# Kernel tuning notes

Measured on AMD Instinct MI355X. Metric: run time of the kernel, lower is better.

The kernel has to match this reference:

```python
import jax, jax.numpy as jnp
import numpy as np

BETA = 0.5
THRESHOLD = 1.0
SLOPE = 25.0  # fast_sigmoid surrogate slope
NUM_STEPS, BATCH = 80, 65536
NUM_INPUTS, NUM_HIDDEN, NUM_OUTPUTS = 20, 10, 2


@jax.custom_vjp
def spike_fn(x):
    # Heaviside fire: spk = 1 if (mem - threshold) > 0
    return (x > 0).astype(x.dtype)

def _spike_fwd(x):
    return spike_fn(x), x

def _spike_bwd(x, g):
    # snntorch surrogate.fast_sigmoid(slope=25): grad = 1/(slope*|x|+1)^2
    return (g / (SLOPE * jnp.abs(x) + 1.0) ** 2,)

spike_fn.defvjp(_spike_fwd, _spike_bwd)


def setup_inputs() -> dict:
    key = jax.random.key(0)
    kx, k1, k2, k3, k4 = jax.random.split(key, 5)
    x = jax.random.normal(kx, (NUM_STEPS, BATCH, NUM_INPUTS), dtype=jnp.float32)
    # nn.Linear-style init: U(-1/sqrt(fan_in), 1/sqrt(fan_in))
    b1_lim = 1.0 / np.sqrt(NUM_INPUTS)
    b2_lim = 1.0 / np.sqrt(NUM_HIDDEN)
    W1 = jax.random.uniform(k1, (NUM_HIDDEN, NUM_INPUTS), jnp.float32, -b1_lim, b1_lim)
    b1 = jax.random.uniform(k2, (NUM_HIDDEN,), jnp.float32, -b1_lim, b1_lim)
    W2 = jax.random.uniform(k3, (NUM_OUTPUTS, NUM_HIDDEN), jnp.float32, -b2_lim, b2_lim)
    b2 = jax.random.uniform(k4, (NUM_OUTPUTS,), jnp.float32, -b2_lim, b2_lim)
    return {"x": x, "W1": W1, "b1": b1, "W2": W2, "b2": b2}


def reference(x, W1, b1, W2, b2):
    B = x.shape[1]
    mem1_0 = jnp.zeros((B, NUM_HIDDEN), dtype=x.dtype)
    mem2_0 = jnp.zeros((B, NUM_OUTPUTS), dtype=x.dtype)

    def step(carry, x_t):
        mem1, mem2 = carry
        # layer 1: Linear + Leaky (reset_mechanism='subtract')
        cur1 = x_t @ W1.T + b1                      # [B, 10]
        reset1 = spike_fn(mem1 - THRESHOLD)         # spike of previous mem
        mem1 = BETA * mem1 + cur1 - reset1 * THRESHOLD
        spk1 = spike_fn(mem1 - THRESHOLD)
        # layer 2
        cur2 = spk1 @ W2.T + b2                     # [B, 2]
        reset2 = spike_fn(mem2 - THRESHOLD)
        mem2 = BETA * mem2 + cur2 - reset2 * THRESHOLD
        spk2 = spike_fn(mem2 - THRESHOLD)
        return (mem1, mem2), (spk2, mem2)

    _, (spk2_rec, mem2_rec) = jax.lax.scan(step, (mem1_0, mem2_0), x)
    return spk2_rec, mem2_rec  # each [80, B, 2]
```

## Files before the change

kernel.cpp:

```cpp
#include <hip/hip_runtime.h>

#define NSTEPS 80
#define BATCH  65536
#define NIN    20
#define NHID   10
#define NOUT   2

__device__ __forceinline__ void load_x20(float* __restrict__ dst,
                                         const float* __restrict__ src) {
#pragma unroll
  for (int k = 0; k < NIN; k += 4) {
    const float4 v = *reinterpret_cast<const float4*>(src + k);
    dst[k + 0] = v.x; dst[k + 1] = v.y; dst[k + 2] = v.z; dst[k + 3] = v.w;
  }
}

__device__ __forceinline__ void st_nt2(float* p, float2 v) {
  union { float2 f; double d; } u; u.f = v;
  __builtin_nontemporal_store(u.d, reinterpret_cast<double*>(p));
}

__device__ __forceinline__ void snn_step(
    const float (&xb)[NIN],
    const float (&w1)[NHID][NIN], const float (&bb1)[NHID],
    const float (&w2)[NOUT][NHID], const float (&bb2)[NOUT],
    float (&mem1)[NHID], float (&mem2)[NOUT],
    float2& spk_out, float2& mem_out)
{
  float spk1[NHID];
#pragma unroll
  for (int j = 0; j < NHID; ++j) {
    float acc = 0.0f;
#pragma unroll
    for (int k = 0; k < NIN; ++k) acc = fmaf(xb[k], w1[j][k], acc);
    const float cur = acc + bb1[j];
    const float reset = (mem1[j] >= 1.0f) ? 1.0f : 0.0f;
    const float m = fmaf(0.5f, mem1[j], cur) - reset;
    mem1[j] = m;
    spk1[j] = (m >= 1.0f) ? 1.0f : 0.0f;
  }
#pragma unroll
  for (int o = 0; o < NOUT; ++o) {
    float acc = 0.0f;
#pragma unroll
    for (int j = 0; j < NHID; ++j) acc = fmaf(spk1[j], w2[o][j], acc);
    const float cur = acc + bb2[o];
    const float reset = (mem2[o] >= 1.0f) ? 1.0f : 0.0f;
    mem2[o] = fmaf(0.5f, mem2[o], cur) - reset;
  }
  spk_out = make_float2((mem2[0] >= 1.0f) ? 1.0f : 0.0f,
                        (mem2[1] >= 1.0f) ? 1.0f : 0.0f);
  mem_out = make_float2(mem2[0], mem2[1]);
}

__global__ __launch_bounds__(256, 1)
void snn_forward(const float* __restrict__ x,
                 const float* __restrict__ W1, const float* __restrict__ B1,
                 const float* __restrict__ W2, const float* __restrict__ B2,
                 float* __restrict__ out)
{
  const int b = blockIdx.x * blockDim.x + threadIdx.x;

  float w1[NHID][NIN];
#pragma unroll
  for (int j = 0; j < NHID; ++j)
#pragma unroll
    for (int k = 0; k < NIN; k += 4) {
      const float4 v = *reinterpret_cast<const float4*>(W1 + j * NIN + k);
      w1[j][k] = v.x; w1[j][k + 1] = v.y; w1[j][k + 2] = v.z; w1[j][k + 3] = v.w;
    }
  float bb1[NHID];
#pragma unroll
  for (int j = 0; j < NHID; ++j) bb1[j] = B1[j];
  float w2[NOUT][NHID];
#pragma unroll
  for (int o = 0; o < NOUT; ++o)
#pragma unroll
    for (int j = 0; j < NHID; ++j) w2[o][j] = W2[o * NHID + j];
  float bb2[NOUT];
#pragma unroll
  for (int o = 0; o < NOUT; ++o) bb2[o] = B2[o];

  float mem1[NHID];
#pragma unroll
  for (int j = 0; j < NHID; ++j) mem1[j] = 0.0f;
  float mem2[NOUT] = {0.0f, 0.0f};

  const size_t ss = (size_t)BATCH * NIN;
  const size_t os = (size_t)BATCH * NOUT;
  const float* xp = x + (size_t)b * NIN;
  float* sp = out + (size_t)b * NOUT;
  float* mp = sp + (size_t)NSTEPS * BATCH * NOUT;

  float B0[NIN], B1b[NIN], B2b[NIN], B3[NIN];
  load_x20(B0,  xp);
  load_x20(B1b, xp + 1 * ss);
  load_x20(B2b, xp + 2 * ss);

#define SNN_STEP_EMIT(BUF)                                          \
  {                                                                 \
    float2 s_, m_;                                                  \
    snn_step(BUF, w1, bb1, w2, bb2, mem1, mem2, s_, m_);            \
    st_nt2(sp, s_); st_nt2(mp, m_);                                 \
    sp += os; mp += os;                                             \
  }

  for (int t = 0; t < NSTEPS; t += 4) {
    if (t + 3 < NSTEPS) load_x20(B3,  xp + (size_t)(t + 3) * ss);
    SNN_STEP_EMIT(B0);
    if (t + 4 < NSTEPS) load_x20(B0,  xp + (size_t)(t + 4) * ss);
    SNN_STEP_EMIT(B1b);
    if (t + 5 < NSTEPS) load_x20(B1b, xp + (size_t)(t + 5) * ss);
    SNN_STEP_EMIT(B2b);
    if (t + 6 < NSTEPS) load_x20(B2b, xp + (size_t)(t + 6) * ss);
    SNN_STEP_EMIT(B3);
  }
#undef SNN_STEP_EMIT
}

extern "C" void kernel_launch(void* const* d_in, const int* in_sizes, int n_in,
                              void* d_out, int out_size, void* d_ws, size_t ws_size,
                              hipStream_t stream) {
  (void)in_sizes; (void)n_in; (void)d_ws; (void)ws_size; (void)out_size;
  const float* x  = (const float*)d_in[0];
  const float* W1 = (const float*)d_in[1];
  const float* B1 = (const float*)d_in[2];
  const float* W2 = (const float*)d_in[3];
  const float* B2 = (const float*)d_in[4];
  float* out = (float*)d_out;

  dim3 grid(BATCH / 256), block(256);
  snn_forward<<<grid, block, 0, stream>>>(x, W1, B1, W2, B2, out);
}
```

Before: 104.4 us.

## Split hidden neurons across lane pairs to double thread count

Each batch element is now handled by two adjacent lanes, each computing five of the ten hidden neurons, exchanging spikes via a lane shuffle. Each lane writes either the spike or membrane output. Doubles the grid and allows two blocks per CU, with a three-buffer prefetch instead of four, to improve latency hiding. Both lanes redundantly load the full input row, and a shuffle per step is added.

```diff
diff --git a/kernel.cpp b/kernel.cpp
--- a/kernel.cpp
+++ b/kernel.cpp
@@ -5,6 +5,7 @@
 #define NIN    20
 #define NHID   10
 #define NOUT   2
+#define NH2    5
 
 __device__ __forceinline__ void load_x20(float* __restrict__ dst,
                                          const float* __restrict__ src) {
@@ -20,30 +21,38 @@
   __builtin_nontemporal_store(u.d, reinterpret_cast<double*>(p));
 }
 
-__device__ __forceinline__ void snn_step(
-    const float (&xb)[NIN],
-    const float (&w1)[NHID][NIN], const float (&bb1)[NHID],
+__device__ __forceinline__ void snn_step2(
+    const float (&xb)[NIN], int h,
+    const float (&w1)[NH2][NIN], const float (&bb1)[NH2],
     const float (&w2)[NOUT][NHID], const float (&bb2)[NOUT],
-    float (&mem1)[NHID], float (&mem2)[NOUT],
+    float (&mem1)[NH2], float (&mem2)[NOUT],
     float2& spk_out, float2& mem_out)
 {
-  float spk1[NHID];
+  float a[NH2];
 #pragma unroll
-  for (int j = 0; j < NHID; ++j) {
+  for (int jj = 0; jj < NH2; ++jj) {
     float acc = 0.0f;
 #pragma unroll
-    for (int k = 0; k < NIN; ++k) acc = fmaf(xb[k], w1[j][k], acc);
-    const float cur = acc + bb1[j];
-    const float reset = (mem1[j] >= 1.0f) ? 1.0f : 0.0f;
-    const float m = fmaf(0.5f, mem1[j], cur) - reset;
-    mem1[j] = m;
-    spk1[j] = (m >= 1.0f) ? 1.0f : 0.0f;
+    for (int k = 0; k < NIN; ++k) acc = fmaf(xb[k], w1[jj][k], acc);
+    const float cur = acc + bb1[jj];
+    const float reset = (mem1[jj] >= 1.0f) ? 1.0f : 0.0f;
+    const float m = fmaf(0.5f, mem1[jj], cur) - reset;
+    mem1[jj] = m;
+    a[jj] = (m >= 1.0f) ? 1.0f : 0.0f;
   }
+  float o5[NH2];
+#pragma unroll
+  for (int jj = 0; jj < NH2; ++jj) o5[jj] = __shfl_xor(a[jj], 1);
+  float s[NHID];
+#pragma unroll
+  for (int j = 0; j < NH2; ++j)  s[j]       = h ? o5[j] : a[j];
+#pragma unroll
+  for (int j = 0; j < NH2; ++j)  s[NH2 + j] = h ? a[j]  : o5[j];
 #pragma unroll
   for (int o = 0; o < NOUT; ++o) {
     float acc = 0.0f;
 #pragma unroll
-    for (int j = 0; j < NHID; ++j) acc = fmaf(spk1[j], w2[o][j], acc);
+    for (int j = 0; j < NHID; ++j) acc = fmaf(s[j], w2[o][j], acc);
     const float cur = acc + bb2[o];
     const float reset = (mem2[o] >= 1.0f) ? 1.0f : 0.0f;
     mem2[o] = fmaf(0.5f, mem2[o], cur) - reset;
@@ -53,25 +62,28 @@
   mem_out = make_float2(mem2[0], mem2[1]);
 }
 
-__global__ __launch_bounds__(256, 1)
-void snn_forward(const float* __restrict__ x,
-                 const float* __restrict__ W1, const float* __restrict__ B1,
-                 const float* __restrict__ W2, const float* __restrict__ B2,
-                 float* __restrict__ out)
+__global__ __launch_bounds__(256, 2)
+void snn_forward2(const float* __restrict__ x,
+                  const float* __restrict__ W1, const float* __restrict__ B1,
+                  const float* __restrict__ W2, const float* __restrict__ B2,
+                  float* __restrict__ out)
 {
-  const int b = blockIdx.x * blockDim.x + threadIdx.x;
+  const int i = blockIdx.x * blockDim.x + threadIdx.x;
+  const int b = i >> 1;
+  const int h = i & 1;
+  const int j0 = NH2 * h;
 
-  float w1[NHID][NIN];
+  float w1[NH2][NIN];
 #pragma unroll
-  for (int j = 0; j < NHID; ++j)
+  for (int jj = 0; jj < NH2; ++jj)
 #pragma unroll
     for (int k = 0; k < NIN; k += 4) {
-      const float4 v = *reinterpret_cast<const float4*>(W1 + j * NIN + k);
-      w1[j][k] = v.x; w1[j][k + 1] = v.y; w1[j][k + 2] = v.z; w1[j][k + 3] = v.w;
+      const float4 v = *reinterpret_cast<const float4*>(W1 + (j0 + jj) * NIN + k);
+      w1[jj][k] = v.x; w1[jj][k + 1] = v.y; w1[jj][k + 2] = v.z; w1[jj][k + 3] = v.w;
     }
-  float bb1[NHID];
+  float bb1[NH2];
 #pragma unroll
-  for (int j = 0; j < NHID; ++j) bb1[j] = B1[j];
+  for (int jj = 0; jj < NH2; ++jj) bb1[jj] = B1[j0 + jj];
   float w2[NOUT][NHID];
 #pragma unroll
   for (int o = 0; o < NOUT; ++o)
@@ -81,40 +93,38 @@
 #pragma unroll
   for (int o = 0; o < NOUT; ++o) bb2[o] = B2[o];
 
-  float mem1[NHID];
+  float mem1[NH2];
 #pragma unroll
-  for (int j = 0; j < NHID; ++j) mem1[j] = 0.0f;
+  for (int jj = 0; jj < NH2; ++jj) mem1[jj] = 0.0f;
   float mem2[NOUT] = {0.0f, 0.0f};
 
   const size_t ss = (size_t)BATCH * NIN;
   const size_t os = (size_t)BATCH * NOUT;
   const float* xp = x + (size_t)b * NIN;
-  float* sp = out + (size_t)b * NOUT;
-  float* mp = sp + (size_t)NSTEPS * BATCH * NOUT;
+  float* op = out + (h ? (size_t)NSTEPS * BATCH * NOUT : 0) + (size_t)b * NOUT;
 
-  float B0[NIN], B1b[NIN], B2b[NIN], B3[NIN];
-  load_x20(B0,  xp);
-  load_x20(B1b, xp + 1 * ss);
-  load_x20(B2b, xp + 2 * ss);
+  float A[NIN], Bb[NIN], C[NIN];
+  load_x20(A,  xp);
+  load_x20(Bb, xp + ss);
 
-#define SNN_STEP_EMIT(BUF)                                          \
-  {                                                                 \
-    float2 s_, m_;                                                  \
-    snn_step(BUF, w1, bb1, w2, bb2, mem1, mem2, s_, m_);            \
-    st_nt2(sp, s_); st_nt2(mp, m_);                                 \
-    sp += os; mp += os;                                             \
+#define SNN_STEP_EMIT(BUF)                                           \
+  {                                                                  \
+    float2 s_, m_;                                                   \
+    snn_step2(BUF, h, w1, bb1, w2, bb2, mem1, mem2, s_, m_);         \
+    st_nt2(op, h ? m_ : s_);                                         \
+    op += os;                                                        \
   }
 
-  for (int t = 0; t < NSTEPS; t += 4) {
-    if (t + 3 < NSTEPS) load_x20(B3,  xp + (size_t)(t + 3) * ss);
-    SNN_STEP_EMIT(B0);
-    if (t + 4 < NSTEPS) load_x20(B0,  xp + (size_t)(t + 4) * ss);
-    SNN_STEP_EMIT(B1b);
-    if (t + 5 < NSTEPS) load_x20(B1b, xp + (size_t)(t + 5) * ss);
-    SNN_STEP_EMIT(B2b);
-    if (t + 6 < NSTEPS) load_x20(B2b, xp + (size_t)(t + 6) * ss);
-    SNN_STEP_EMIT(B3);
+  for (int t = 0; t < 78; t += 3) {
+    load_x20(C,  xp + (size_t)(t + 2) * ss);
+    SNN_STEP_EMIT(A);
+    load_x20(A,  xp + (size_t)(t + 3) * ss);
+    SNN_STEP_EMIT(Bb);
+    load_x20(Bb, xp + (size_t)(t + 4) * ss);
+    SNN_STEP_EMIT(C);
   }
+  SNN_STEP_EMIT(A);
+  SNN_STEP_EMIT(Bb);
 #undef SNN_STEP_EMIT
 }
 
@@ -129,6 +139,6 @@
   const float* B2 = (const float*)d_in[4];
   float* out = (float*)d_out;
 
-  dim3 grid(BATCH / 256), block(256);
-  snn_forward<<<grid, block, 0, stream>>>(x, W1, B1, W2, B2, out);
+  dim3 grid(2 * BATCH / 256), block(256);
+  snn_forward2<<<grid, block, 0, stream>>>(x, W1, B1, W2, B2, out);
 }
```

Measured after the change: 99.92 us. -4.3%, faster.

## Split each batch row across a quad of lanes with shuffle-based exchange

Applied to the files above, without the earlier changes.

Each batch element is now handled by four lanes. Each lane loads a float4 slice of the input, and the quad all-gathers the slices via xor shuffles. Each lane computes three of the ten hidden neurons and the spikes are exchanged by shuffles. Moving W1 into shared memory, giving each lane fewer registers and launching four times as many threads are meant to raise occupancy and memory-level parallelism. In exchange, the shuffles and the layer-2 computation are duplicated across the quad, and lane q==0 does extra work on the tail elements.

```diff
diff --git a/kernel.cpp b/kernel.cpp
--- a/kernel.cpp
+++ b/kernel.cpp
@@ -6,116 +6,161 @@
 #define NHID   10
 #define NOUT   2
 
-__device__ __forceinline__ void load_x20(float* __restrict__ dst,
-                                         const float* __restrict__ src) {
-#pragma unroll
-  for (int k = 0; k < NIN; k += 4) {
-    const float4 v = *reinterpret_cast<const float4*>(src + k);
-    dst[k + 0] = v.x; dst[k + 1] = v.y; dst[k + 2] = v.z; dst[k + 3] = v.w;
-  }
-}
-
 __device__ __forceinline__ void st_nt2(float* p, float2 v) {
   union { float2 f; double d; } u; u.f = v;
   __builtin_nontemporal_store(u.d, reinterpret_cast<double*>(p));
 }
 
-__device__ __forceinline__ void snn_step(
-    const float (&xb)[NIN],
-    const float (&w1)[NHID][NIN], const float (&bb1)[NHID],
-    const float (&w2)[NOUT][NHID], const float (&bb2)[NOUT],
-    float (&mem1)[NHID], float (&mem2)[NOUT],
-    float2& spk_out, float2& mem_out)
-{
-  float spk1[NHID];
+__device__ __constant__ int c_row0[4] = {0, 3, 6, 8};
+
+__device__ __forceinline__ void quad_allgather4(float (&G)[4][4],
+                                                const float4 V, int q) {
+  float v[4] = {V.x, V.y, V.z, V.w};
+  float u[4], p[4], w[4];
 #pragma unroll
-  for (int j = 0; j < NHID; ++j) {
-    float acc = 0.0f;
+  for (int c = 0; c < 4; ++c) u[c] = __shfl_xor(v[c], 1);
 #pragma unroll
-    for (int k = 0; k < NIN; ++k) acc = fmaf(xb[k], w1[j][k], acc);
-    const float cur = acc + bb1[j];
-    const float reset = (mem1[j] >= 1.0f) ? 1.0f : 0.0f;
-    const float m = fmaf(0.5f, mem1[j], cur) - reset;
-    mem1[j] = m;
-    spk1[j] = (m >= 1.0f) ? 1.0f : 0.0f;
+  for (int c = 0; c < 4; ++c) p[c] = __shfl_xor(v[c], 2);
+#pragma unroll
+  for (int c = 0; c < 4; ++c) w[c] = __shfl_xor(u[c], 2);
+#pragma unroll
+  for (int a = 0; a < 4; ++a) {
+#pragma unroll
+    for (int c = 0; c < 4; ++c) {
+      const int m = q ^ a;
+      G[a][c] = (m == 0) ? v[c] : (m == 1) ? u[c] : (m == 2) ? p[c] : w[c];
+    }
   }
-#pragma unroll
-  for (int o = 0; o < NOUT; ++o) {
-    float acc = 0.0f;
-#pragma unroll
-    for (int j = 0; j < NHID; ++j) acc = fmaf(spk1[j], w2[o][j], acc);
-    const float cur = acc + bb2[o];
-    const float reset = (mem2[o] >= 1.0f) ? 1.0f : 0.0f;
-    mem2[o] = fmaf(0.5f, mem2[o], cur) - reset;
-  }
-  spk_out = make_float2((mem2[0] >= 1.0f) ? 1.0f : 0.0f,
-                        (mem2[1] >= 1.0f) ? 1.0f : 0.0f);
-  mem_out = make_float2(mem2[0], mem2[1]);
 }
 
-__global__ __launch_bounds__(256, 1)
-void snn_forward(const float* __restrict__ x,
-                 const float* __restrict__ W1, const float* __restrict__ B1,
-                 const float* __restrict__ W2, const float* __restrict__ B2,
-                 float* __restrict__ out)
+__global__ __launch_bounds__(256, 4)
+void snn_forward4(const float* __restrict__ x,
+                  const float* __restrict__ W1, const float* __restrict__ B1,
+                  const float* __restrict__ W2, const float* __restrict__ B2,
+                  float* __restrict__ out)
 {
-  const int b = blockIdx.x * blockDim.x + threadIdx.x;
+  __shared__ float sw1[NHID][NIN];
+  const int tid = threadIdx.x;
+  if (tid < NHID * NIN) sw1[tid / NIN][tid % NIN] = W1[tid];
+  __syncthreads();
 
-  float w1[NHID][NIN];
-#pragma unroll
-  for (int j = 0; j < NHID; ++j)
-#pragma unroll
-    for (int k = 0; k < NIN; k += 4) {
-      const float4 v = *reinterpret_cast<const float4*>(W1 + j * NIN + k);
-      w1[j][k] = v.x; w1[j][k + 1] = v.y; w1[j][k + 2] = v.z; w1[j][k + 3] = v.w;
-    }
-  float bb1[NHID];
-#pragma unroll
-  for (int j = 0; j < NHID; ++j) bb1[j] = B1[j];
+  const int i = blockIdx.x * blockDim.x + tid;
+  const int b = i >> 2;
+  const int q = i & 3;
+  const int r0 = c_row0[q];
+  const int r1 = r0 + 1;
+  const int r2 = (q < 2) ? (r0 + 2) : 9;
+
+  float bb1[3];
+  bb1[0] = B1[r0]; bb1[1] = B1[r1]; bb1[2] = B1[r2];
   float w2[NOUT][NHID];
 #pragma unroll
   for (int o = 0; o < NOUT; ++o)
 #pragma unroll
     for (int j = 0; j < NHID; ++j) w2[o][j] = W2[o * NHID + j];
-  float bb2[NOUT];
-#pragma unroll
-  for (int o = 0; o < NOUT; ++o) bb2[o] = B2[o];
+  float bb2[NOUT] = {B2[0], B2[1]};
 
-  float mem1[NHID];
-#pragma unroll
-  for (int j = 0; j < NHID; ++j) mem1[j] = 0.0f;
+  float mem1[3] = {0.0f, 0.0f, 0.0f};
   float mem2[NOUT] = {0.0f, 0.0f};
 
   const size_t ss = (size_t)BATCH * NIN;
   const size_t os = (size_t)BATCH * NOUT;
-  const float* xp = x + (size_t)b * NIN;
-  float* sp = out + (size_t)b * NOUT;
-  float* mp = sp + (size_t)NSTEPS * BATCH * NOUT;
+  const float* xp = x + (size_t)b * NIN + 4 * q;
+  const float* xt = x + (size_t)b * NIN + 16;
+  float* op = out + (q ? (size_t)NSTEPS * BATCH * NOUT : 0) + (size_t)b * NOUT;
 
-  float B0[NIN], B1b[NIN], B2b[NIN], B3[NIN];
-  load_x20(B0,  xp);
-  load_x20(B1b, xp + 1 * ss);
-  load_x20(B2b, xp + 2 * ss);
+  float4 VA, VB, TA, TB;
+  VA = *reinterpret_cast<const float4*>(xp);
+  if (q == 0) TA = *reinterpret_cast<const float4*>(xt);
+  VB = *reinterpret_cast<const float4*>(xp + ss);
+  if (q == 0) TB = *reinterpret_cast<const float4*>(xt + ss);
 
-#define SNN_STEP_EMIT(BUF)                                          \
-  {                                                                 \
-    float2 s_, m_;                                                  \
-    snn_step(BUF, w1, bb1, w2, bb2, mem1, mem2, s_, m_);            \
-    st_nt2(sp, s_); st_nt2(mp, m_);                                 \
-    sp += os; mp += os;                                             \
+#define SNN_STEP(VW, TW)                                                     \
+  {                                                                          \
+        \
+    float G[4][4];                                                           \
+    quad_allgather4(G, VW, q);                                               \
+    float xb[NIN];                                                           \
+    _Pragma("unroll")                                                        \
+    for (int a = 0; a < 4; ++a)                                              \
+      _Pragma("unroll")                                                      \
+      for (int c = 0; c < 4; ++c) xb[4 * a + c] = G[a][c];                   \
+    {                                                                        \
+      float tv[4] = {TW.x, TW.y, TW.z, TW.w};                                \
+      float t1[4], t2[4], t3[4];                                             \
+      _Pragma("unroll")                                                      \
+      for (int c = 0; c < 4; ++c) t1[c] = __shfl_xor(tv[c], 1);              \
+      _Pragma("unroll")                                                      \
+      for (int c = 0; c < 4; ++c) t2[c] = __shfl_xor(tv[c], 2);              \
+      _Pragma("unroll")                                                      \
+      for (int c = 0; c < 4; ++c) t3[c] = __shfl_xor(t1[c], 2);              \
+      _Pragma("unroll")                                                      \
+      for (int c = 0; c < 4; ++c)                                            \
+        xb[16 + c] = (q == 0) ? tv[c] : (q == 1) ? t1[c]                     \
+                   : (q == 2) ? t2[c] : t3[c];                               \
+    }                                                                        \
+           \
+    float sp[3];                                                             \
+    const int rows[3] = {r0, r1, r2};                                        \
+    _Pragma("unroll")                                                        \
+    for (int n = 0; n < 3; ++n) {                                            \
+      float acc = 0.0f;                                                      \
+      _Pragma("unroll")                                                      \
+      for (int k = 0; k < NIN; ++k) acc = fmaf(xb[k], sw1[rows[n]][k], acc); \
+      const float cur = acc + bb1[n];                                        \
+      const float reset = (mem1[n] >= 1.0f) ? 1.0f : 0.0f;                   \
+      const float m = fmaf(0.5f, mem1[n], cur) - reset;                      \
+      mem1[n] = m;                                                           \
+      sp[n] = (m >= 1.0f) ? 1.0f : 0.0f;                                     \
+    }                                                                        \
+                     \
+    float su[3], sP[3], sw_[3];                                              \
+    _Pragma("unroll")                                                        \
+    for (int n = 0; n < 3; ++n) su[n] = __shfl_xor(sp[n], 1);                \
+    _Pragma("unroll")                                                        \
+    for (int n = 0; n < 3; ++n) sP[n] = __shfl_xor(sp[n], 2);                \
+    _Pragma("unroll")                                                        \
+    for (int n = 0; n < 3; ++n) sw_[n] = __shfl_xor(su[n], 2);               \
+    float s[NHID];                                                           \
+    _Pragma("unroll")                                                        \
+    for (int j = 0; j < NHID; ++j) {                                         \
+      const int qs = (j < 3) ? 0 : (j < 6) ? 1 : (j < 8) ? 2 : 3;            \
+      const int n  = (j < 3) ? j : (j < 6) ? j - 3 : (j < 8) ? j - 6 : j - 8;\
+      const int m  = q ^ qs;                                                 \
+      s[j] = (m == 0) ? sp[n] : (m == 1) ? su[n] : (m == 2) ? sP[n] : sw_[n];\
+    }                                                                        \
+                                        \
+    _Pragma("unroll")                                                        \
+    for (int o = 0; o < NOUT; ++o) {                                         \
+      float acc = 0.0f;                                                      \
+      _Pragma("unroll")                                                      \
+      for (int j = 0; j < NHID; ++j) acc = fmaf(s[j], w2[o][j], acc);        \
+      const float cur = acc + bb2[o];                                        \
+      const float reset = (mem2[o] >= 1.0f) ? 1.0f : 0.0f;                   \
+      mem2[o] = fmaf(0.5f, mem2[o], cur) - reset;                            \
+    }                                                                        \
+    if (q < 2) {                                                             \
+      const float2 v = q ? make_float2(mem2[0], mem2[1])                     \
+                         : make_float2((mem2[0] >= 1.0f) ? 1.0f : 0.0f,      \
+                                       (mem2[1] >= 1.0f) ? 1.0f : 0.0f);     \
+      st_nt2(op, v);                                                         \
+    }                                                                        \
+    op += os;                                                                \
   }
 
-  for (int t = 0; t < NSTEPS; t += 4) {
-    if (t + 3 < NSTEPS) load_x20(B3,  xp + (size_t)(t + 3) * ss);
-    SNN_STEP_EMIT(B0);
-    if (t + 4 < NSTEPS) load_x20(B0,  xp + (size_t)(t + 4) * ss);
-    SNN_STEP_EMIT(B1b);
-    if (t + 5 < NSTEPS) load_x20(B1b, xp + (size_t)(t + 5) * ss);
-    SNN_STEP_EMIT(B2b);
-    if (t + 6 < NSTEPS) load_x20(B2b, xp + (size_t)(t + 6) * ss);
-    SNN_STEP_EMIT(B3);
+  for (int t = 0; t < NSTEPS; t += 2) {
+    SNN_STEP(VA, TA);
+    if (t + 2 < NSTEPS) {
+      VA = *reinterpret_cast<const float4*>(xp + (size_t)(t + 2) * ss);
+      if (q == 0) TA = *reinterpret_cast<const float4*>(xt + (size_t)(t + 2) * ss);
+    }
+    SNN_STEP(VB, TB);
+    if (t + 3 < NSTEPS) {
+      VB = *reinterpret_cast<const float4*>(xp + (size_t)(t + 3) * ss);
+      if (q == 0) TB = *reinterpret_cast<const float4*>(xt + (size_t)(t + 3) * ss);
+    }
   }
-#undef SNN_STEP_EMIT
+#undef SNN_STEP
 }
 
 extern "C" void kernel_launch(void* const* d_in, const int* in_sizes, int n_in,
@@ -129,6 +174,6 @@
   const float* B2 = (const float*)d_in[4];
   float* out = (float*)d_out;
 
-  dim3 grid(BATCH / 256), block(256);
-  snn_forward<<<grid, block, 0, stream>>>(x, W1, B1, W2, B2, out);
+  dim3 grid(4 * BATCH / 256), block(256);
+  snn_forward4<<<grid, block, 0, stream>>>(x, W1, B1, W2, B2, out);
 }
```

After: 392.3 us. +275.7%, slower.
